# Performance work log

Measured on AMD Instinct MI355X. Metric: run time of the kernel, lower is better.

The kernel has to match this reference:

```python
import math
import jax, jax.numpy as jnp
import numpy as np

B, Q, K, D = 32, 1024, 1024, 128
MASK_VALUE = -1000000.0


def setup_inputs() -> dict:
    key = jax.random.key(0)
    kq, kk, kv, kl = jax.random.split(key, 4)
    return {
        "queries": jax.random.normal(kq, (B, Q, D), dtype=jnp.float32),
        "keys": jax.random.normal(kk, (B, K, D), dtype=jnp.float32),
        "values": jax.random.normal(kv, (B, K, D), dtype=jnp.float32),
        "valid_lens": jax.random.randint(kl, (B,), 1, K + 1, dtype=jnp.int32),
    }


def reference(queries, keys, values, valid_lens):
    d = queries.shape[-1]
    # scores: [B, Q, K]
    scores = jnp.einsum("bqd,bkd->bqk", queries, keys) / math.sqrt(d)
    # key-padding mask: position k valid iff k < valid_lens[b] (broadcast over queries)
    mask = jnp.arange(keys.shape[1])[None, None, :] < valid_lens[:, None, None]
    scores = jnp.where(mask, scores, MASK_VALUE)
    attn = jax.nn.softmax(scores, axis=-1)
    # dropout p=0.0 -> identity
    return jnp.einsum("bqk,bkv->bqv", attn, values)
```

## Files before the change

kernel.cpp:

```cpp
#include <hip/hip_runtime.h>
#include <math.h>

typedef _Float16 f16;
typedef __attribute__((ext_vector_type(8))) _Float16 f16x8;
typedef __attribute__((ext_vector_type(4))) _Float16 f16x4;
typedef __attribute__((ext_vector_type(4))) float f32x4;

constexpr int BATCH = 32;
constexpr int QL = 1024;
constexpr int KL = 1024;
constexpr int D = 128;
constexpr int BQ = 128;
constexpr int BK = 64;
constexpr int DKP = 136;
constexpr int BKP = 72;

#define CSC 0.12752863187087177f

static __device__ __forceinline__ f16x4 pk4(float x, float y, float z, float w) {
  auto a = __builtin_amdgcn_cvt_pkrtz(x, y);
  auto b = __builtin_amdgcn_cvt_pkrtz(z, w);
  f16x4 h;
  h[0] = (f16)a[0]; h[1] = (f16)a[1]; h[2] = (f16)b[0]; h[3] = (f16)b[1];
  return h;
}
static __device__ __forceinline__ f16x8 pk8(float4 u, float4 v) {
  f16x4 a = pk4(u.x, u.y, u.z, u.w);
  f16x4 b = pk4(v.x, v.y, v.z, v.w);
  f16x8 h;
  h[0] = a[0]; h[1] = a[1]; h[2] = a[2]; h[3] = a[3];
  h[4] = b[0]; h[5] = b[1]; h[6] = b[2]; h[7] = b[3];
  return h;
}
static __device__ __forceinline__ f16x8 pk8v(f32x4 a, f32x4 b) {
  auto x0 = __builtin_amdgcn_cvt_pkrtz(a[0], a[1]);
  auto x1 = __builtin_amdgcn_cvt_pkrtz(a[2], a[3]);
  auto x2 = __builtin_amdgcn_cvt_pkrtz(b[0], b[1]);
  auto x3 = __builtin_amdgcn_cvt_pkrtz(b[2], b[3]);
  f16x8 h;
  h[0] = x0[0]; h[1] = x0[1]; h[2] = x1[0]; h[3] = x1[1];
  h[4] = x2[0]; h[5] = x2[1]; h[6] = x3[0]; h[7] = x3[1];
  return h;
}
static __device__ __forceinline__ f16x8 pk8s(float4 u, float4 v) {
  float4 a = {u.x * CSC, u.y * CSC, u.z * CSC, u.w * CSC};
  float4 b = {v.x * CSC, v.y * CSC, v.z * CSC, v.w * CSC};
  return pk8(a, b);
}

static __device__ __forceinline__ int krp(int kk) {
  return ((kk >> 5) << 5) | (((kk >> 2) & 1) << 4) | (((kk >> 3) & 3) << 2) | (kk & 3);
}

#define ISSUE(KR, VR, T)                                                   \
  do {                                                                     \
    const float4* Kt = (const float4*)(Kb + (size_t)(T) * BK * D);         \
    _Pragma("unroll")                                                      \
    for (int i_ = 0; i_ < 4; ++i_) {                                       \
      int cc_ = tid + i_ * 256;                                            \
      int row_ = cc_ >> 4, d04_ = (cc_ & 15) * 2;                          \
      KR[2 * i_]     = Kt[row_ * 32 + d04_];                               \
      KR[2 * i_ + 1] = Kt[row_ * 32 + d04_ + 1];                           \
    }                                                                      \
    const float* Vt = Vb + (size_t)(T) * BK * D;                           \
    _Pragma("unroll")                                                      \
    for (int i_ = 0; i_ < 2; ++i_) {                                       \
      int f_ = tid + i_ * 256;                                             \
      const float* base_ = Vt + (size_t)((f_ & 15) * 4) * D + (f_ >> 4) * 4; \
      VR[i_ * 4 + 0] = *(const float4*)(base_);                            \
      VR[i_ * 4 + 1] = *(const float4*)(base_ + D);                        \
      VR[i_ * 4 + 2] = *(const float4*)(base_ + 2 * D);                    \
      VR[i_ * 4 + 3] = *(const float4*)(base_ + 3 * D);                    \
    }                                                                      \
  } while (0)

#define DRAIN(KR, VR, NB)                                                  \
  do {                                                                     \
    _Pragma("unroll")                                                      \
    for (int i_ = 0; i_ < 4; ++i_) {                                       \
      int cc_ = tid + i_ * 256;                                            \
      int row_ = cc_ >> 4, d0_ = (cc_ & 15) * 8;                           \
      *(f16x8*)&sK[NB][krp(row_)][d0_] = pk8(KR[2 * i_], KR[2 * i_ + 1]);  \
    }                                                                      \
    _Pragma("unroll")                                                      \
    for (int i_ = 0; i_ < 2; ++i_) {                                       \
      int f_ = tid + i_ * 256;                                             \
      int k0_ = (f_ & 15) * 4, d0_ = (f_ >> 4) * 4;                        \
      float4 r0_ = VR[i_*4+0], r1_ = VR[i_*4+1], r2_ = VR[i_*4+2], r3_ = VR[i_*4+3]; \
      *(f16x4*)&sVT[NB][d0_ + 0][k0_] = pk4(r0_.x, r1_.x, r2_.x, r3_.x);   \
      *(f16x4*)&sVT[NB][d0_ + 1][k0_] = pk4(r0_.y, r1_.y, r2_.y, r3_.y);   \
      *(f16x4*)&sVT[NB][d0_ + 2][k0_] = pk4(r0_.z, r1_.z, r2_.z, r3_.z);   \
      *(f16x4*)&sVT[NB][d0_ + 3][k0_] = pk4(r0_.w, r1_.w, r2_.w, r3_.w);   \
    }                                                                      \
  } while (0)

#define TILE_BARRIER()                                                     \
  do {                                                                     \
    asm volatile("s_waitcnt lgkmcnt(0)" ::: "memory");                     \
    __builtin_amdgcn_s_barrier();                                          \
    asm volatile("" ::: "memory");                                         \
  } while (0)

#define SOFTMAX_HALF(SV, MM, LL, PF, OO)                                   \
  do {                                                                     \
    float t0_ = fmaxf(fmaxf(SV[0][0], SV[0][1]), fmaxf(SV[0][2], SV[0][3]));\
    float t1_ = fmaxf(fmaxf(SV[1][0], SV[1][1]), fmaxf(SV[1][2], SV[1][3]));\
    float t2_ = fmaxf(fmaxf(SV[2][0], SV[2][1]), fmaxf(SV[2][2], SV[2][3]));\
    float t3_ = fmaxf(fmaxf(SV[3][0], SV[3][1]), fmaxf(SV[3][2], SV[3][3]));\
    float pmax_ = fmaxf(fmaxf(t0_, t1_), fmaxf(t2_, t3_));                 \
    pmax_ = fmaxf(pmax_, __shfl_xor(pmax_, 16));                           \
    pmax_ = fmaxf(pmax_, __shfl_xor(pmax_, 32));                           \
    float mnew_  = fmaxf(MM, pmax_);                                       \
    float alpha_ = __builtin_amdgcn_exp2f(MM - mnew_);                     \
    MM = mnew_;                                                            \
    float ls_ = 0.f;                                                       \
    _Pragma("unroll")                                                      \
    for (int ct_ = 0; ct_ < 4; ++ct_) {                                    \
      _Pragma("unroll")                                                    \
      for (int r_ = 0; r_ < 4; ++r_) {                                     \
        float p_ = __builtin_amdgcn_exp2f(SV[ct_][r_] - mnew_);            \
        SV[ct_][r_] = p_;                                                  \
        ls_ += p_;                                                         \
      }                                                                    \
    }                                                                      \
    ls_ += __shfl_xor(ls_, 16);                                            \
    ls_ += __shfl_xor(ls_, 32);                                            \
    LL = LL * alpha_ + ls_;                                                \
    PF[0] = pk8v(SV[0], SV[1]);                                            \
    PF[1] = pk8v(SV[2], SV[3]);                                            \
    _Pragma("unroll")                                                      \
    for (int dt_ = 0; dt_ < 8; ++dt_) OO[dt_] *= alpha_;                   \
  } while (0)

__global__ __launch_bounds__(256, 1)
void attn_fwd(const float* __restrict__ Qp, const float* __restrict__ Kp,
              const float* __restrict__ Vp, const int* __restrict__ VLp,
              float* __restrict__ Op) {
  __shared__ f16 sK[2][BK][DKP];
  __shared__ f16 sVT[2][D][BKP];
  __shared__ int sN[32];
  __shared__ int sI[32];

  const int tid  = threadIdx.x;
  const int wave = tid >> 6, lane = tid & 63;
  const int l16  = lane & 15, quad = lane >> 4;

  if (tid < 32) sN[tid] = (VLp[tid] + BK - 1) / BK;
  __syncthreads();
  if (tid < 32) {
    int nb = sN[tid], r = 0;
    #pragma unroll
    for (int k = 0; k < 32; ++k) {
      int nk = sN[k];
      r += (nk > nb) || (nk == nb && k < tid);
    }
    sI[r] = tid;
  }
  __syncthreads();
  const int xcd = blockIdx.x & 7;
  const int j   = (int)blockIdx.x >> 3;
  const int lr  = j >> 3;
  const int qt  = j & 7;
  const int grank = (lr == 0) ? xcd : (lr == 1) ? (15 - xcd)
                  : (lr == 2) ? (16 + xcd) : (31 - xcd);
  const int b  = sI[grank];
  const int vl = VLp[b];

  const float* Kb = Kp + (size_t)b * KL * D;
  const float* Vb = Vp + (size_t)b * KL * D;
  const int ntiles = (vl + BK - 1) / BK;

  float4 kreg[8], vreg[8];

  const float* Qb = Qp + ((size_t)(b * QL + qt * BQ + wave * 32 + l16)) * D;
  float4 qtmp[16];
  #pragma unroll
  for (int h = 0; h < 2; ++h)
    #pragma unroll
    for (int kc = 0; kc < 4; ++kc) {
      const float* p = Qb + h * 16 * D + kc * 32 + quad * 8;
      qtmp[h * 8 + 2 * kc]     = *(const float4*)p;
      qtmp[h * 8 + 2 * kc + 1] = *(const float4*)(p + 4);
    }

  ISSUE(kreg, vreg, 0);

  f16x8 qf0[4], qf1[4];
  #pragma unroll
  for (int kc = 0; kc < 4; ++kc)
    qf0[kc] = pk8s(qtmp[2 * kc], qtmp[2 * kc + 1]);
  #pragma unroll
  for (int kc = 0; kc < 4; ++kc)
    qf1[kc] = pk8s(qtmp[8 + 2 * kc], qtmp[8 + 2 * kc + 1]);

  float m0 = -INFINITY, m1 = -INFINITY;
  float l0 = 0.f, l1 = 0.f;
  f32x4 o0[8], o1[8];
  #pragma unroll
  for (int dt = 0; dt < 8; ++dt) {
    o0[dt] = (f32x4){0.f, 0.f, 0.f, 0.f};
    o1[dt] = (f32x4){0.f, 0.f, 0.f, 0.f};
  }

  DRAIN(kreg, vreg, 0);
  TILE_BARRIER();

  for (int t = 0; t < ntiles; ++t) {
    const int cur = t & 1, nxt = cur ^ 1;
    const bool more = (t + 1 < ntiles);

    if (more) ISSUE(kreg, vreg, t + 1);

    f32x4 s0[4], s1[4];
    #pragma unroll
    for (int ct = 0; ct < 4; ++ct) {
      s0[ct] = (f32x4){0.f, 0.f, 0.f, 0.f};
      s1[ct] = (f32x4){0.f, 0.f, 0.f, 0.f};
      #pragma unroll
      for (int kc = 0; kc < 4; ++kc) {
        f16x8 kf = *(const f16x8*)&sK[cur][ct * 16 + l16][kc * 32 + quad * 8];
        s0[ct] = __builtin_amdgcn_mfma_f32_16x16x32_f16(kf, qf0[kc], s0[ct], 0, 0, 0);
        s1[ct] = __builtin_amdgcn_mfma_f32_16x16x32_f16(kf, qf1[kc], s1[ct], 0, 0, 0);
      }
    }

    if (t * BK + BK > vl) {
      #pragma unroll
      for (int ct = 0; ct < 4; ++ct) {
        int kb = t * BK + (ct >> 1) * 32 + (ct & 1) * 4 + quad * 8;
        #pragma unroll
        for (int r = 0; r < 4; ++r) {
          bool ok = (kb + r) < vl;
          s0[ct][r] = ok ? s0[ct][r] : -1.0e9f;
          s1[ct][r] = ok ? s1[ct][r] : -1.0e9f;
        }
      }
    }

    f16x8 pf0[2], pf1[2];
    SOFTMAX_HALF(s0, m0, l0, pf0, o0);
    SOFTMAX_HALF(s1, m1, l1, pf1, o1);

    #pragma unroll
    for (int ks = 0; ks < 2; ++ks) {
      #pragma unroll
      for (int dt = 0; dt < 8; ++dt) {
        f16x8 vf = *(const f16x8*)&sVT[cur][dt * 16 + l16][ks * 32 + quad * 8];
        o0[dt] = __builtin_amdgcn_mfma_f32_16x16x32_f16(vf, pf0[ks], o0[dt], 0, 0, 0);
        o1[dt] = __builtin_amdgcn_mfma_f32_16x16x32_f16(vf, pf1[ks], o1[dt], 0, 0, 0);
      }
    }

    if (more) DRAIN(kreg, vreg, nxt);
    TILE_BARRIER();
  }

  float* Ob = Op + ((size_t)(b * QL + qt * BQ + wave * 32)) * D;
  const float inv0 = 1.0f / l0, inv1 = 1.0f / l1;
  #pragma unroll
  for (int dt = 0; dt < 8; ++dt) {
    float4 w0 = {o0[dt][0] * inv0, o0[dt][1] * inv0, o0[dt][2] * inv0, o0[dt][3] * inv0};
    float4 w1 = {o1[dt][0] * inv1, o1[dt][1] * inv1, o1[dt][2] * inv1, o1[dt][3] * inv1};
    *(float4*)&Ob[(size_t)l16 * D + dt * 16 + quad * 4]        = w0;
    *(float4*)&Ob[(size_t)(16 + l16) * D + dt * 16 + quad * 4] = w1;
  }
}

extern "C" void kernel_launch(void* const* d_in, const int* in_sizes, int n_in,
                              void* d_out, int out_size, void* d_ws, size_t ws_size,
                              hipStream_t stream) {
  const float* Qp = (const float*)d_in[0];
  const float* Kp = (const float*)d_in[1];
  const float* Vp = (const float*)d_in[2];
  const int*   VL = (const int*)d_in[3];
  float* Op = (float*)d_out;

  attn_fwd<<<dim3(QL / BQ * BATCH), dim3(256), 0, stream>>>(Qp, Kp, Vp, VL, Op);
}
```

Baseline: 126.7 us.

## Halve query tile to 64 rows with one row-group per wave and two blocks per CU

The query tile shrinks from 128 to 64 rows, so each wave handles 16 query rows instead of 32. The two-half softmax and accumulator sets collapse into one, and launch bounds allow two blocks per CU. The block-to-batch mapping is also changed to a folded order over the doubled grid to balance variable-length batches across XCDs. The goal is more resident waves and better latency hiding. The cost is that each K/V tile loaded into shared memory is reused by half as many queries, which doubles K/V traffic and conversion work.

```diff
diff --git a/kernel.cpp b/kernel.cpp
--- a/kernel.cpp
+++ b/kernel.cpp
@@ -10,7 +10,7 @@
 constexpr int QL = 1024;
 constexpr int KL = 1024;
 constexpr int D = 128;
-constexpr int BQ = 128;
+constexpr int BQ = 64;
 constexpr int BK = 64;
 constexpr int DKP = 136;
 constexpr int BKP = 72;
@@ -101,38 +101,7 @@
     asm volatile("" ::: "memory");                                         \
   } while (0)
 
-#define SOFTMAX_HALF(SV, MM, LL, PF, OO)                                   \
-  do {                                                                     \
-    float t0_ = fmaxf(fmaxf(SV[0][0], SV[0][1]), fmaxf(SV[0][2], SV[0][3]));\
-    float t1_ = fmaxf(fmaxf(SV[1][0], SV[1][1]), fmaxf(SV[1][2], SV[1][3]));\
-    float t2_ = fmaxf(fmaxf(SV[2][0], SV[2][1]), fmaxf(SV[2][2], SV[2][3]));\
-    float t3_ = fmaxf(fmaxf(SV[3][0], SV[3][1]), fmaxf(SV[3][2], SV[3][3]));\
-    float pmax_ = fmaxf(fmaxf(t0_, t1_), fmaxf(t2_, t3_));                 \
-    pmax_ = fmaxf(pmax_, __shfl_xor(pmax_, 16));                           \
-    pmax_ = fmaxf(pmax_, __shfl_xor(pmax_, 32));                           \
-    float mnew_  = fmaxf(MM, pmax_);                                       \
-    float alpha_ = __builtin_amdgcn_exp2f(MM - mnew_);                     \
-    MM = mnew_;                                                            \
-    float ls_ = 0.f;                                                       \
-    _Pragma("unroll")                                                      \
-    for (int ct_ = 0; ct_ < 4; ++ct_) {                                    \
-      _Pragma("unroll")                                                    \
-      for (int r_ = 0; r_ < 4; ++r_) {                                     \
-        float p_ = __builtin_amdgcn_exp2f(SV[ct_][r_] - mnew_);            \
-        SV[ct_][r_] = p_;                                                  \
-        ls_ += p_;                                                         \
-      }                                                                    \
-    }                                                                      \
-    ls_ += __shfl_xor(ls_, 16);                                            \
-    ls_ += __shfl_xor(ls_, 32);                                            \
-    LL = LL * alpha_ + ls_;                                                \
-    PF[0] = pk8v(SV[0], SV[1]);                                            \
-    PF[1] = pk8v(SV[2], SV[3]);                                            \
-    _Pragma("unroll")                                                      \
-    for (int dt_ = 0; dt_ < 8; ++dt_) OO[dt_] *= alpha_;                   \
-  } while (0)
-
-__global__ __launch_bounds__(256, 1)
+__global__ __launch_bounds__(256, 2)
 void attn_fwd(const float* __restrict__ Qp, const float* __restrict__ Kp,
               const float* __restrict__ Vp, const int* __restrict__ VLp,
               float* __restrict__ Op) {
@@ -159,8 +128,9 @@
   __syncthreads();
   const int xcd = blockIdx.x & 7;
   const int j   = (int)blockIdx.x >> 3;
-  const int lr  = j >> 3;
-  const int qt  = j & 7;
+  const int jj  = (j < 32) ? j : (95 - j);
+  const int lr  = jj >> 4;
+  const int qt  = jj & 15;
   const int grank = (lr == 0) ? xcd : (lr == 1) ? (15 - xcd)
                   : (lr == 2) ? (16 + xcd) : (31 - xcd);
   const int b  = sI[grank];
@@ -172,35 +142,25 @@
 
   float4 kreg[8], vreg[8];
 
-  const float* Qb = Qp + ((size_t)(b * QL + qt * BQ + wave * 32 + l16)) * D;
-  float4 qtmp[16];
-  #pragma unroll
-  for (int h = 0; h < 2; ++h)
-    #pragma unroll
-    for (int kc = 0; kc < 4; ++kc) {
-      const float* p = Qb + h * 16 * D + kc * 32 + quad * 8;
-      qtmp[h * 8 + 2 * kc]     = *(const float4*)p;
-      qtmp[h * 8 + 2 * kc + 1] = *(const float4*)(p + 4);
-    }
+  const float* Qb = Qp + ((size_t)(b * QL + qt * BQ + wave * 16 + l16)) * D;
+  float4 qtmp[8];
+  #pragma unroll
+  for (int kc = 0; kc < 4; ++kc) {
+    const float* p = Qb + kc * 32 + quad * 8;
+    qtmp[2 * kc]     = *(const float4*)p;
+    qtmp[2 * kc + 1] = *(const float4*)(p + 4);
+  }
 
   ISSUE(kreg, vreg, 0);
 
-  f16x8 qf0[4], qf1[4];
-  #pragma unroll
-  for (int kc = 0; kc < 4; ++kc)
-    qf0[kc] = pk8s(qtmp[2 * kc], qtmp[2 * kc + 1]);
-  #pragma unroll
-  for (int kc = 0; kc < 4; ++kc)
-    qf1[kc] = pk8s(qtmp[8 + 2 * kc], qtmp[8 + 2 * kc + 1]);
-
-  float m0 = -INFINITY, m1 = -INFINITY;
-  float l0 = 0.f, l1 = 0.f;
-  f32x4 o0[8], o1[8];
-  #pragma unroll
-  for (int dt = 0; dt < 8; ++dt) {
-    o0[dt] = (f32x4){0.f, 0.f, 0.f, 0.f};
-    o1[dt] = (f32x4){0.f, 0.f, 0.f, 0.f};
-  }
+  f16x8 qf[4];
+  #pragma unroll
+  for (int kc = 0; kc < 4; ++kc) qf[kc] = pk8s(qtmp[2 * kc], qtmp[2 * kc + 1]);
+
+  float m2 = -INFINITY, lsum = 0.f;
+  f32x4 o[8];
+  #pragma unroll
+  for (int dt = 0; dt < 8; ++dt) o[dt] = (f32x4){0.f, 0.f, 0.f, 0.f};
 
   DRAIN(kreg, vreg, 0);
   TILE_BARRIER();
@@ -211,17 +171,16 @@
 
     if (more) ISSUE(kreg, vreg, t + 1);
 
-    f32x4 s0[4], s1[4];
+    f32x4 sv[4];
     #pragma unroll
     for (int ct = 0; ct < 4; ++ct) {
-      s0[ct] = (f32x4){0.f, 0.f, 0.f, 0.f};
-      s1[ct] = (f32x4){0.f, 0.f, 0.f, 0.f};
+      f32x4 cacc = (f32x4){0.f, 0.f, 0.f, 0.f};
       #pragma unroll
       for (int kc = 0; kc < 4; ++kc) {
         f16x8 kf = *(const f16x8*)&sK[cur][ct * 16 + l16][kc * 32 + quad * 8];
-        s0[ct] = __builtin_amdgcn_mfma_f32_16x16x32_f16(kf, qf0[kc], s0[ct], 0, 0, 0);
-        s1[ct] = __builtin_amdgcn_mfma_f32_16x16x32_f16(kf, qf1[kc], s1[ct], 0, 0, 0);
+        cacc = __builtin_amdgcn_mfma_f32_16x16x32_f16(kf, qf[kc], cacc, 0, 0, 0);
       }
+      sv[ct] = cacc;
     }
 
     if (t * BK + BK > vl) {
@@ -229,40 +188,59 @@
       for (int ct = 0; ct < 4; ++ct) {
         int kb = t * BK + (ct >> 1) * 32 + (ct & 1) * 4 + quad * 8;
         #pragma unroll
+        for (int r = 0; r < 4; ++r)
+          sv[ct][r] = (kb + r) < vl ? sv[ct][r] : -1.0e9f;
+      }
+    }
+
+    {
+      float t0 = fmaxf(fmaxf(sv[0][0], sv[0][1]), fmaxf(sv[0][2], sv[0][3]));
+      float t1 = fmaxf(fmaxf(sv[1][0], sv[1][1]), fmaxf(sv[1][2], sv[1][3]));
+      float t2 = fmaxf(fmaxf(sv[2][0], sv[2][1]), fmaxf(sv[2][2], sv[2][3]));
+      float t3 = fmaxf(fmaxf(sv[3][0], sv[3][1]), fmaxf(sv[3][2], sv[3][3]));
+      float pmax = fmaxf(fmaxf(t0, t1), fmaxf(t2, t3));
+      pmax = fmaxf(pmax, __shfl_xor(pmax, 16));
+      pmax = fmaxf(pmax, __shfl_xor(pmax, 32));
+      float mnew  = fmaxf(m2, pmax);
+      float alpha = __builtin_amdgcn_exp2f(m2 - mnew);
+      m2 = mnew;
+      float ls = 0.f;
+      #pragma unroll
+      for (int ct = 0; ct < 4; ++ct) {
+        #pragma unroll
         for (int r = 0; r < 4; ++r) {
-          bool ok = (kb + r) < vl;
-          s0[ct][r] = ok ? s0[ct][r] : -1.0e9f;
-          s1[ct][r] = ok ? s1[ct][r] : -1.0e9f;
+          float p = __builtin_amdgcn_exp2f(sv[ct][r] - mnew);
+          sv[ct][r] = p;
+          ls += p;
         }
       }
-    }
-
-    f16x8 pf0[2], pf1[2];
-    SOFTMAX_HALF(s0, m0, l0, pf0, o0);
-    SOFTMAX_HALF(s1, m1, l1, pf1, o1);
+      ls += __shfl_xor(ls, 16);
+      ls += __shfl_xor(ls, 32);
+      lsum = lsum * alpha + ls;
+      #pragma unroll
+      for (int dt = 0; dt < 8; ++dt) o[dt] *= alpha;
+    }
+    f16x8 pf0 = pk8v(sv[0], sv[1]);
+    f16x8 pf1 = pk8v(sv[2], sv[3]);
 
     #pragma unroll
-    for (int ks = 0; ks < 2; ++ks) {
-      #pragma unroll
-      for (int dt = 0; dt < 8; ++dt) {
-        f16x8 vf = *(const f16x8*)&sVT[cur][dt * 16 + l16][ks * 32 + quad * 8];
-        o0[dt] = __builtin_amdgcn_mfma_f32_16x16x32_f16(vf, pf0[ks], o0[dt], 0, 0, 0);
-        o1[dt] = __builtin_amdgcn_mfma_f32_16x16x32_f16(vf, pf1[ks], o1[dt], 0, 0, 0);
-      }
+    for (int dt = 0; dt < 8; ++dt) {
+      f16x8 vf0 = *(const f16x8*)&sVT[cur][dt * 16 + l16][quad * 8];
+      o[dt] = __builtin_amdgcn_mfma_f32_16x16x32_f16(vf0, pf0, o[dt], 0, 0, 0);
+      f16x8 vf1 = *(const f16x8*)&sVT[cur][dt * 16 + l16][32 + quad * 8];
+      o[dt] = __builtin_amdgcn_mfma_f32_16x16x32_f16(vf1, pf1, o[dt], 0, 0, 0);
     }
 
     if (more) DRAIN(kreg, vreg, nxt);
     TILE_BARRIER();
   }
 
-  float* Ob = Op + ((size_t)(b * QL + qt * BQ + wave * 32)) * D;
-  const float inv0 = 1.0f / l0, inv1 = 1.0f / l1;
+  float* Ob = Op + ((size_t)(b * QL + qt * BQ + wave * 16)) * D;
+  const float inv = 1.0f / lsum;
   #pragma unroll
   for (int dt = 0; dt < 8; ++dt) {
-    float4 w0 = {o0[dt][0] * inv0, o0[dt][1] * inv0, o0[dt][2] * inv0, o0[dt][3] * inv0};
-    float4 w1 = {o1[dt][0] * inv1, o1[dt][1] * inv1, o1[dt][2] * inv1, o1[dt][3] * inv1};
-    *(float4*)&Ob[(size_t)l16 * D + dt * 16 + quad * 4]        = w0;
-    *(float4*)&Ob[(size_t)(16 + l16) * D + dt * 16 + quad * 4] = w1;
+    float4 w = {o[dt][0] * inv, o[dt][1] * inv, o[dt][2] * inv, o[dt][3] * inv};
+    *(float4*)&Ob[(size_t)l16 * D + dt * 16 + quad * 4] = w;
   }
 }
 
```

Result: faster. 115.9 us (-8.5%).
